# Performance work log

Hardware: AMD Instinct MI355X
Metric: run time of the kernel (lower is better)

Reference implementation:

```python
import jax, jax.numpy as jnp
import numpy as np
import math

GH, GW = 64, 64
FEAT_DIM = 32
NUM_COMP = 8
N = 1_000_000
H1, H2 = 128, 64
TWO_PI = 2.0 * math.pi
LN_EPS = 1e-5


def _layernorm(h, g, b):
    mu = jnp.mean(h, axis=-1, keepdims=True)
    var = jnp.var(h, axis=-1, keepdims=True)
    return (h - mu) * jax.lax.rsqrt(var + LN_EPS) * g + b


def setup_inputs() -> dict:
    key = jax.random.key(0)
    ks = jax.random.split(key, 8)
    coords = jax.random.uniform(ks[0], (N, 2), dtype=jnp.float32)
    feature_grid = jax.random.normal(ks[1], (GH, GW, FEAT_DIM), dtype=jnp.float32)
    d_in = 2 + FEAT_DIM
    W1 = jax.random.normal(ks[2], (d_in, H1), dtype=jnp.float32) / np.sqrt(d_in)
    b1 = jnp.zeros((H1,), jnp.float32)
    g1 = jnp.ones((H1,), jnp.float32)
    be1 = jnp.zeros((H1,), jnp.float32)
    W2 = jax.random.normal(ks[3], (H1, H2), dtype=jnp.float32) / np.sqrt(H1)
    b2 = jnp.zeros((H2,), jnp.float32)
    g2 = jnp.ones((H2,), jnp.float32)
    be2 = jnp.zeros((H2,), jnp.float32)
    W3 = jax.random.normal(ks[4], (H2, 6 * NUM_COMP), dtype=jnp.float32) / np.sqrt(H2)
    b3 = jnp.zeros((6 * NUM_COMP,), jnp.float32)
    return {"coords": coords, "feature_grid": feature_grid,
            "W1": W1, "b1": b1, "g1": g1, "be1": be1,
            "W2": W2, "b2": b2, "g2": g2, "be2": be2,
            "W3": W3, "b3": b3}


def reference(coords, feature_grid, W1, b1, g1, be1, W2, b2, g2, be2, W3, b3):
    # bilinear gather from feature grid
    x = coords[:, 0] * (GW - 1)
    y = coords[:, 1] * (GH - 1)
    x0 = jnp.clip(jnp.floor(x).astype(jnp.int32), 0, GW - 2)
    y0 = jnp.clip(jnp.floor(y).astype(jnp.int32), 0, GH - 2)
    x1 = x0 + 1
    y1 = y0 + 1
    dx = (x - x0.astype(jnp.float32))[:, None]
    dy = (y - y0.astype(jnp.float32))[:, None]
    f00 = feature_grid[y0, x0]  # [N, F]
    f01 = feature_grid[y1, x0]
    f10 = feature_grid[y0, x1]
    f11 = feature_grid[y1, x1]
    feat = ((1 - dx) * (1 - dy) * f00 + (1 - dx) * dy * f01
            + dx * (1 - dy) * f10 + dx * dy * f11)
    # MLP (dropout is identity in eval mode)
    h = jnp.concatenate([coords, feat], axis=-1)
    h = _layernorm(jax.nn.relu(h @ W1 + b1), g1, be1)
    h = _layernorm(jax.nn.relu(h @ W2 + b2), g2, be2)
    params = (h @ W3 + b3).reshape(-1, NUM_COMP, 6)
    # GMM parameter postprocessing
    weights = jax.nn.softmax(params[:, :, 0], axis=-1)
    speed = jax.nn.relu(params[:, :, 1])
    angle = jnp.mod(params[:, :, 2], TWO_PI)
    variances = jnp.exp(jnp.clip(params[:, :, 3:5], -10.0, 10.0))
    corr = 0.99 * jnp.tanh(params[:, :, 5])
    means = jnp.stack([speed, angle], axis=-1)
    gmm = jnp.concatenate([weights[..., None], means, variances, corr[..., None]], axis=-1)
    return (gmm, coords)
```

## Files before the change

kernel.cpp:

```cpp
#include <hip/hip_runtime.h>
#include <math.h>


constexpr int N_PTS = 1000000;
constexpr int GW = 64;
constexpr int FDIM = 32;
constexpr int DIN = 34;
constexpr int NH1 = 128;
constexpr int NH2 = 64;
constexpr int NOUT = 48;
constexpr int NC = 8;
constexpr int BLK = 128;

template<int N>
__device__ __forceinline__ float np_pairwise(const float* x) {
#pragma clang fp contract(off)
    float r[8];
#pragma unroll
    for (int j = 0; j < 8; ++j) r[j] = x[j];
#pragma unroll
    for (int m = 1; m < N / 8; ++m)
#pragma unroll
        for (int j = 0; j < 8; ++j) r[j] = r[j] + x[8 * m + j];
    return ((r[0] + r[1]) + (r[2] + r[3])) + ((r[4] + r[5]) + (r[6] + r[7]));
}

template<int N>
__device__ __forceinline__ float np_pairwise_sq(const float* x, float mu) {
#pragma clang fp contract(off)
    float r[8];
#pragma unroll
    for (int j = 0; j < 8; ++j) { const float d = x[j] - mu; r[j] = d * d; }
#pragma unroll
    for (int m = 1; m < N / 8; ++m)
#pragma unroll
        for (int j = 0; j < 8; ++j) {
            const float d = x[8 * m + j] - mu;
            r[j] = r[j] + d * d;
        }
    return ((r[0] + r[1]) + (r[2] + r[3])) + ((r[4] + r[5]) + (r[6] + r[7]));
}

__global__ __launch_bounds__(BLK, 2) void modgmm_np32(
    const float* __restrict__ coords,
    const float* __restrict__ grid,
    const float* __restrict__ W1, const float* __restrict__ b1,
    const float* __restrict__ g1, const float* __restrict__ be1,
    const float* __restrict__ W2, const float* __restrict__ b2,
    const float* __restrict__ g2, const float* __restrict__ be2,
    const float* __restrict__ W3, const float* __restrict__ b3,
    float* __restrict__ gmm_out, float* __restrict__ coords_out)
{
#pragma clang fp contract(off)
    __shared__ float sbuf[64 * BLK];
    const int tid = threadIdx.x;
    const int i = blockIdx.x * BLK + tid;
    if (i >= N_PTS) return;

    const float2 c2 = reinterpret_cast<const float2*>(coords)[i];
    const float cx = c2.x, cy = c2.y;

    const float x = cx * 63.0f;
    const float y = cy * 63.0f;
    int x0 = (int)floorf(x); x0 = x0 < 0 ? 0 : (x0 > 62 ? 62 : x0);
    int y0 = (int)floorf(y); y0 = y0 < 0 ? 0 : (y0 > 62 ? 62 : y0);
    const float dx = x - (float)x0;
    const float dy = y - (float)y0;
    const float omdx = 1.0f - dx;
    const float omdy = 1.0f - dy;
    const float w00 = omdx * omdy;
    const float w01 = omdx * dy;
    const float w10 = dx * omdy;
    const float w11 = dx * dy;

    const float* __restrict__ gp = grid + (y0 * GW + x0) * FDIM;

    sbuf[0 * BLK + tid] = cx;
    sbuf[1 * BLK + tid] = cy;
#pragma unroll
    for (int k = 0; k < FDIM; ++k) {
        const float t0 = w00 * gp[k];
        const float t1 = w01 * gp[GW * FDIM + k];
        const float t2 = w10 * gp[FDIM + k];
        const float t3 = w11 * gp[GW * FDIM + FDIM + k];
        sbuf[(2 + k) * BLK + tid] = ((t0 + t1) + t2) + t3;
    }

    float h[NH1];
#pragma unroll
    for (int j = 0; j < NH1; ++j) h[j] = 0.0f;
    for (int k = 0; k < DIN; ++k) {
        const float hv = sbuf[k * BLK + tid];
        const float* __restrict__ wr = W1 + k * NH1;
#pragma unroll
        for (int j = 0; j < NH1; ++j) h[j] = __builtin_fmaf(hv, wr[j], h[j]);
    }
#pragma unroll
    for (int j = 0; j < NH1; ++j) h[j] = fmaxf(h[j] + b1[j], 0.0f);

    {
        const float mu = np_pairwise<NH1>(h) / 128.0f;
        const float var = np_pairwise_sq<NH1>(h, mu) / 128.0f;
        const float rs = 1.0f / sqrtf(var + 1e-5f);
#pragma unroll
        for (int j = 0; j < NH1; ++j)
            h[j] = ((h[j] - mu) * rs) * g1[j] + be1[j];
    }

    float h2[NH2];
#pragma unroll
    for (int j = 0; j < NH2; ++j) h2[j] = 0.0f;
#pragma unroll
    for (int j = 0; j < 64; ++j) sbuf[j * BLK + tid] = h[j];
    for (int k = 0; k < 64; ++k) {
        const float hv = sbuf[k * BLK + tid];
        const float* __restrict__ wr = W2 + k * NH2;
#pragma unroll
        for (int j = 0; j < NH2; ++j) h2[j] = __builtin_fmaf(hv, wr[j], h2[j]);
    }
#pragma unroll
    for (int j = 0; j < 64; ++j) sbuf[j * BLK + tid] = h[64 + j];
    for (int k = 0; k < 64; ++k) {
        const float hv = sbuf[k * BLK + tid];
        const float* __restrict__ wr = W2 + (64 + k) * NH2;
#pragma unroll
        for (int j = 0; j < NH2; ++j) h2[j] = __builtin_fmaf(hv, wr[j], h2[j]);
    }
#pragma unroll
    for (int j = 0; j < NH2; ++j) h2[j] = fmaxf(h2[j] + b2[j], 0.0f);

    {
        const float mu = np_pairwise<NH2>(h2) / 64.0f;
        const float var = np_pairwise_sq<NH2>(h2, mu) / 64.0f;
        const float rs = 1.0f / sqrtf(var + 1e-5f);
#pragma unroll
        for (int j = 0; j < NH2; ++j)
            h2[j] = ((h2[j] - mu) * rs) * g2[j] + be2[j];
    }

    float o[NOUT];
#pragma unroll
    for (int j = 0; j < NOUT; ++j) o[j] = 0.0f;
#pragma unroll
    for (int j = 0; j < NH2; ++j) sbuf[j * BLK + tid] = h2[j];
    for (int k = 0; k < NH2; ++k) {
        const float hv = sbuf[k * BLK + tid];
        const float* __restrict__ wr = W3 + k * NOUT;
#pragma unroll
        for (int j = 0; j < NOUT; ++j) o[j] = __builtin_fmaf(hv, wr[j], o[j]);
    }
#pragma unroll
    for (int j = 0; j < NOUT; ++j) o[j] = o[j] + b3[j];

    const float TPf = 6.28318530717958647692f;
    float res[NOUT];
    float m = o[0];
#pragma unroll
    for (int c = 1; c < NC; ++c) m = fmaxf(m, o[6 * c]);
    float e[NC];
#pragma unroll
    for (int c = 0; c < NC; ++c) e[c] = expf(o[6 * c] - m);
    const float esum = ((e[0] + e[1]) + (e[2] + e[3])) + ((e[4] + e[5]) + (e[6] + e[7]));
#pragma unroll
    for (int c = 0; c < NC; ++c) {
        res[6 * c + 0] = e[c] / esum;
        res[6 * c + 1] = fmaxf(o[6 * c + 1], 0.0f);
        float a = fmodf(o[6 * c + 2], TPf);
        if (a < 0.0f) a += TPf;
        res[6 * c + 2] = a;
        res[6 * c + 3] = expf(fminf(fmaxf(o[6 * c + 3], -10.0f), 10.0f));
        res[6 * c + 4] = expf(fminf(fmaxf(o[6 * c + 4], -10.0f), 10.0f));
        res[6 * c + 5] = 0.99f * tanhf(o[6 * c + 5]);
    }

    float4* og = reinterpret_cast<float4*>(gmm_out + (size_t)i * NOUT);
#pragma unroll
    for (int q = 0; q < NOUT / 4; ++q)
        og[q] = make_float4(res[4 * q + 0], res[4 * q + 1], res[4 * q + 2], res[4 * q + 3]);
    reinterpret_cast<float2*>(coords_out)[i] = make_float2(cx, cy);
}

extern "C" void kernel_launch(void* const* d_in, const int* in_sizes, int n_in,
                              void* d_out, int out_size, void* d_ws, size_t ws_size,
                              hipStream_t stream) {
    const float* coords = (const float*)d_in[0];
    const float* grid   = (const float*)d_in[1];
    const float* W1  = (const float*)d_in[2];
    const float* b1  = (const float*)d_in[3];
    const float* g1  = (const float*)d_in[4];
    const float* be1 = (const float*)d_in[5];
    const float* W2  = (const float*)d_in[6];
    const float* b2  = (const float*)d_in[7];
    const float* g2  = (const float*)d_in[8];
    const float* be2 = (const float*)d_in[9];
    const float* W3  = (const float*)d_in[10];
    const float* b3  = (const float*)d_in[11];

    float* gmm_out    = (float*)d_out;
    float* coords_out = (float*)d_out + (size_t)N_PTS * NOUT;

    const int nblocks = (N_PTS + BLK - 1) / BLK;
    modgmm_np32<<<nblocks, BLK, 0, stream>>>(
        coords, grid, W1, b1, g1, be1, W2, b2, g2, be2, W3, b3,
        gmm_out, coords_out);
}
```

Baseline: 563.6 us.

## Split each point's MLP across four lanes with LDS exchange and shuffles

Each point is now handled by four lanes of the same wavefront. Every lane computes a quarter of each layer's outputs using float4 weight loads, writes it to LDS, and all four lanes read back the full row for the layer norm and the next layer. The softmax over the 8 components is finished with cross-lane xor shuffles. The goal is to cut per-thread register pressure (32/16/12 accumulators instead of 128/64/48) and so raise occupancy and latency hiding. In exchange, weight loads are no longer uniform across the wave, so they cannot use scalar loads. The layer-norm statistics are also recomputed redundantly by all four lanes, and the LDS exchange relies on wave-synchronous execution with no barrier.

```diff
diff --git a/kernel.cpp b/kernel.cpp
--- a/kernel.cpp
+++ b/kernel.cpp
@@ -9,39 +9,10 @@
 constexpr int NH1 = 128;
 constexpr int NH2 = 64;
 constexpr int NOUT = 48;
-constexpr int NC = 8;
-constexpr int BLK = 128;
-
-template<int N>
-__device__ __forceinline__ float np_pairwise(const float* x) {
-#pragma clang fp contract(off)
-    float r[8];
-#pragma unroll
-    for (int j = 0; j < 8; ++j) r[j] = x[j];
-#pragma unroll
-    for (int m = 1; m < N / 8; ++m)
-#pragma unroll
-        for (int j = 0; j < 8; ++j) r[j] = r[j] + x[8 * m + j];
-    return ((r[0] + r[1]) + (r[2] + r[3])) + ((r[4] + r[5]) + (r[6] + r[7]));
-}
-
-template<int N>
-__device__ __forceinline__ float np_pairwise_sq(const float* x, float mu) {
-#pragma clang fp contract(off)
-    float r[8];
-#pragma unroll
-    for (int j = 0; j < 8; ++j) { const float d = x[j] - mu; r[j] = d * d; }
-#pragma unroll
-    for (int m = 1; m < N / 8; ++m)
-#pragma unroll
-        for (int j = 0; j < 8; ++j) {
-            const float d = x[8 * m + j] - mu;
-            r[j] = r[j] + d * d;
-        }
-    return ((r[0] + r[1]) + (r[2] + r[3])) + ((r[4] + r[5]) + (r[6] + r[7]));
-}
-
-__global__ __launch_bounds__(BLK, 2) void modgmm_np32(
+constexpr int BLK = 256;
+constexpr int PTS = 64;
+
+__global__ __launch_bounds__(BLK, 4) void modgmm_np32_split4(
     const float* __restrict__ coords,
     const float* __restrict__ grid,
     const float* __restrict__ W1, const float* __restrict__ b1,
@@ -52,14 +23,16 @@
     float* __restrict__ gmm_out, float* __restrict__ coords_out)
 {
 #pragma clang fp contract(off)
-    __shared__ float sbuf[64 * BLK];
-    const int tid = threadIdx.x;
-    const int i = blockIdx.x * BLK + tid;
-    if (i >= N_PTS) return;
-
-    const float2 c2 = reinterpret_cast<const float2*>(coords)[i];
+    __shared__ float buf[NH1 * PTS];
+    const int tid  = threadIdx.x;
+    const int lane = tid & 63;
+    const int g    = lane >> 4;
+    const int pt   = ((tid >> 6) << 4) + (lane & 15);
+    const int gi   = blockIdx.x * PTS + pt;
+#define BUF(r) buf[(r) * PTS + pt]
+
+    const float2 c2 = reinterpret_cast<const float2*>(coords)[gi];
     const float cx = c2.x, cy = c2.y;
-
     const float x = cx * 63.0f;
     const float y = cy * 63.0f;
     int x0 = (int)floorf(x); x0 = x0 < 0 ? 0 : (x0 > 62 ? 62 : x0);
@@ -73,111 +46,215 @@
     const float w10 = dx * omdy;
     const float w11 = dx * dy;
 
-    const float* __restrict__ gp = grid + (y0 * GW + x0) * FDIM;
-
-    sbuf[0 * BLK + tid] = cx;
-    sbuf[1 * BLK + tid] = cy;
-#pragma unroll
-    for (int k = 0; k < FDIM; ++k) {
-        const float t0 = w00 * gp[k];
-        const float t1 = w01 * gp[GW * FDIM + k];
-        const float t2 = w10 * gp[FDIM + k];
-        const float t3 = w11 * gp[GW * FDIM + FDIM + k];
-        sbuf[(2 + k) * BLK + tid] = ((t0 + t1) + t2) + t3;
-    }
-
-    float h[NH1];
-#pragma unroll
-    for (int j = 0; j < NH1; ++j) h[j] = 0.0f;
+    if (g == 0) { BUF(0) = cx; BUF(1) = cy; }
+
+    {
+        const float* gp = grid + (y0 * GW + x0) * FDIM + g * 8;
+        const float4* q00 = reinterpret_cast<const float4*>(gp);
+        const float4* q01 = reinterpret_cast<const float4*>(gp + GW * FDIM);
+        const float4* q10 = reinterpret_cast<const float4*>(gp + FDIM);
+        const float4* q11 = reinterpret_cast<const float4*>(gp + GW * FDIM + FDIM);
+#pragma unroll
+        for (int e = 0; e < 2; ++e) {
+            const float4 a = q00[e], b = q01[e], c = q10[e], d = q11[e];
+            const int r = 2 + g * 8 + e * 4;
+            { const float t0 = w00*a.x, t1 = w01*b.x, t2 = w10*c.x, t3 = w11*d.x;
+              BUF(r+0) = ((t0 + t1) + t2) + t3; }
+            { const float t0 = w00*a.y, t1 = w01*b.y, t2 = w10*c.y, t3 = w11*d.y;
+              BUF(r+1) = ((t0 + t1) + t2) + t3; }
+            { const float t0 = w00*a.z, t1 = w01*b.z, t2 = w10*c.z, t3 = w11*d.z;
+              BUF(r+2) = ((t0 + t1) + t2) + t3; }
+            { const float t0 = w00*a.w, t1 = w01*b.w, t2 = w10*c.w, t3 = w11*d.w;
+              BUF(r+3) = ((t0 + t1) + t2) + t3; }
+        }
+    }
+
+    float acc[32];
+#pragma unroll
+    for (int jj = 0; jj < 32; ++jj) acc[jj] = 0.0f;
     for (int k = 0; k < DIN; ++k) {
-        const float hv = sbuf[k * BLK + tid];
-        const float* __restrict__ wr = W1 + k * NH1;
-#pragma unroll
-        for (int j = 0; j < NH1; ++j) h[j] = __builtin_fmaf(hv, wr[j], h[j]);
-    }
-#pragma unroll
-    for (int j = 0; j < NH1; ++j) h[j] = fmaxf(h[j] + b1[j], 0.0f);
-
-    {
-        const float mu = np_pairwise<NH1>(h) / 128.0f;
-        const float var = np_pairwise_sq<NH1>(h, mu) / 128.0f;
-        const float rs = 1.0f / sqrtf(var + 1e-5f);
-#pragma unroll
-        for (int j = 0; j < NH1; ++j)
-            h[j] = ((h[j] - mu) * rs) * g1[j] + be1[j];
-    }
-
-    float h2[NH2];
-#pragma unroll
-    for (int j = 0; j < NH2; ++j) h2[j] = 0.0f;
-#pragma unroll
-    for (int j = 0; j < 64; ++j) sbuf[j * BLK + tid] = h[j];
-    for (int k = 0; k < 64; ++k) {
-        const float hv = sbuf[k * BLK + tid];
-        const float* __restrict__ wr = W2 + k * NH2;
-#pragma unroll
-        for (int j = 0; j < NH2; ++j) h2[j] = __builtin_fmaf(hv, wr[j], h2[j]);
-    }
-#pragma unroll
-    for (int j = 0; j < 64; ++j) sbuf[j * BLK + tid] = h[64 + j];
-    for (int k = 0; k < 64; ++k) {
-        const float hv = sbuf[k * BLK + tid];
-        const float* __restrict__ wr = W2 + (64 + k) * NH2;
-#pragma unroll
-        for (int j = 0; j < NH2; ++j) h2[j] = __builtin_fmaf(hv, wr[j], h2[j]);
-    }
-#pragma unroll
-    for (int j = 0; j < NH2; ++j) h2[j] = fmaxf(h2[j] + b2[j], 0.0f);
-
-    {
-        const float mu = np_pairwise<NH2>(h2) / 64.0f;
-        const float var = np_pairwise_sq<NH2>(h2, mu) / 64.0f;
-        const float rs = 1.0f / sqrtf(var + 1e-5f);
-#pragma unroll
-        for (int j = 0; j < NH2; ++j)
-            h2[j] = ((h2[j] - mu) * rs) * g2[j] + be2[j];
-    }
-
-    float o[NOUT];
-#pragma unroll
-    for (int j = 0; j < NOUT; ++j) o[j] = 0.0f;
-#pragma unroll
-    for (int j = 0; j < NH2; ++j) sbuf[j * BLK + tid] = h2[j];
+        const float hv = BUF(k);
+        const float4* w4 = reinterpret_cast<const float4*>(W1 + k * NH1 + g * 32);
+#pragma unroll
+        for (int q = 0; q < 8; ++q) {
+            const float4 w = w4[q];
+            acc[4*q+0] = __builtin_fmaf(hv, w.x, acc[4*q+0]);
+            acc[4*q+1] = __builtin_fmaf(hv, w.y, acc[4*q+1]);
+            acc[4*q+2] = __builtin_fmaf(hv, w.z, acc[4*q+2]);
+            acc[4*q+3] = __builtin_fmaf(hv, w.w, acc[4*q+3]);
+        }
+    }
+    {
+        const float4* bv4 = reinterpret_cast<const float4*>(b1 + g * 32);
+#pragma unroll
+        for (int q = 0; q < 8; ++q) {
+            const float4 bv = bv4[q];
+            acc[4*q+0] = fmaxf(acc[4*q+0] + bv.x, 0.0f);
+            acc[4*q+1] = fmaxf(acc[4*q+1] + bv.y, 0.0f);
+            acc[4*q+2] = fmaxf(acc[4*q+2] + bv.z, 0.0f);
+            acc[4*q+3] = fmaxf(acc[4*q+3] + bv.w, 0.0f);
+        }
+#pragma unroll
+        for (int jj = 0; jj < 32; ++jj) BUF(g * 32 + jj) = acc[jj];
+    }
+
+    float mu1, rs1;
+    {
+        float r[8];
+#pragma unroll
+        for (int j = 0; j < 8; ++j) r[j] = BUF(j);
+#pragma unroll
+        for (int m = 1; m < 16; ++m)
+#pragma unroll
+            for (int j = 0; j < 8; ++j) r[j] = r[j] + BUF(8 * m + j);
+        mu1 = (((r[0]+r[1]) + (r[2]+r[3])) + ((r[4]+r[5]) + (r[6]+r[7]))) / 128.0f;
+#pragma unroll
+        for (int j = 0; j < 8; ++j) { const float d = BUF(j) - mu1; r[j] = d * d; }
+#pragma unroll
+        for (int m = 1; m < 16; ++m)
+#pragma unroll
+            for (int j = 0; j < 8; ++j) {
+                const float d = BUF(8 * m + j) - mu1;
+                r[j] = r[j] + d * d;
+            }
+        const float var = (((r[0]+r[1]) + (r[2]+r[3])) + ((r[4]+r[5]) + (r[6]+r[7]))) / 128.0f;
+        rs1 = 1.0f / sqrtf(var + 1e-5f);
+    }
+    {
+        const float4* gv4 = reinterpret_cast<const float4*>(g1 + g * 32);
+        const float4* ev4 = reinterpret_cast<const float4*>(be1 + g * 32);
+#pragma unroll
+        for (int q = 0; q < 8; ++q) {
+            const float4 gv = gv4[q], ev = ev4[q];
+            BUF(g*32 + 4*q+0) = ((acc[4*q+0] - mu1) * rs1) * gv.x + ev.x;
+            BUF(g*32 + 4*q+1) = ((acc[4*q+1] - mu1) * rs1) * gv.y + ev.y;
+            BUF(g*32 + 4*q+2) = ((acc[4*q+2] - mu1) * rs1) * gv.z + ev.z;
+            BUF(g*32 + 4*q+3) = ((acc[4*q+3] - mu1) * rs1) * gv.w + ev.w;
+        }
+    }
+
+    float acc2[16];
+#pragma unroll
+    for (int jj = 0; jj < 16; ++jj) acc2[jj] = 0.0f;
+    for (int k = 0; k < NH1; ++k) {
+        const float hv = BUF(k);
+        const float4* w4 = reinterpret_cast<const float4*>(W2 + k * NH2 + g * 16);
+#pragma unroll
+        for (int q = 0; q < 4; ++q) {
+            const float4 w = w4[q];
+            acc2[4*q+0] = __builtin_fmaf(hv, w.x, acc2[4*q+0]);
+            acc2[4*q+1] = __builtin_fmaf(hv, w.y, acc2[4*q+1]);
+            acc2[4*q+2] = __builtin_fmaf(hv, w.z, acc2[4*q+2]);
+            acc2[4*q+3] = __builtin_fmaf(hv, w.w, acc2[4*q+3]);
+        }
+    }
+    {
+        const float4* bv4 = reinterpret_cast<const float4*>(b2 + g * 16);
+#pragma unroll
+        for (int q = 0; q < 4; ++q) {
+            const float4 bv = bv4[q];
+            acc2[4*q+0] = fmaxf(acc2[4*q+0] + bv.x, 0.0f);
+            acc2[4*q+1] = fmaxf(acc2[4*q+1] + bv.y, 0.0f);
+            acc2[4*q+2] = fmaxf(acc2[4*q+2] + bv.z, 0.0f);
+            acc2[4*q+3] = fmaxf(acc2[4*q+3] + bv.w, 0.0f);
+        }
+#pragma unroll
+        for (int jj = 0; jj < 16; ++jj) BUF(g * 16 + jj) = acc2[jj];
+    }
+
+    float mu2, rs2;
+    {
+        float r[8];
+#pragma unroll
+        for (int j = 0; j < 8; ++j) r[j] = BUF(j);
+#pragma unroll
+        for (int m = 1; m < 8; ++m)
+#pragma unroll
+            for (int j = 0; j < 8; ++j) r[j] = r[j] + BUF(8 * m + j);
+        mu2 = (((r[0]+r[1]) + (r[2]+r[3])) + ((r[4]+r[5]) + (r[6]+r[7]))) / 64.0f;
+#pragma unroll
+        for (int j = 0; j < 8; ++j) { const float d = BUF(j) - mu2; r[j] = d * d; }
+#pragma unroll
+        for (int m = 1; m < 8; ++m)
+#pragma unroll
+            for (int j = 0; j < 8; ++j) {
+                const float d = BUF(8 * m + j) - mu2;
+                r[j] = r[j] + d * d;
+            }
+        const float var = (((r[0]+r[1]) + (r[2]+r[3])) + ((r[4]+r[5]) + (r[6]+r[7]))) / 64.0f;
+        rs2 = 1.0f / sqrtf(var + 1e-5f);
+    }
+    {
+        const float4* gv4 = reinterpret_cast<const float4*>(g2 + g * 16);
+        const float4* ev4 = reinterpret_cast<const float4*>(be2 + g * 16);
+#pragma unroll
+        for (int q = 0; q < 4; ++q) {
+            const float4 gv = gv4[q], ev = ev4[q];
+            BUF(g*16 + 4*q+0) = ((acc2[4*q+0] - mu2) * rs2) * gv.x + ev.x;
+            BUF(g*16 + 4*q+1) = ((acc2[4*q+1] - mu2) * rs2) * gv.y + ev.y;
+            BUF(g*16 + 4*q+2) = ((acc2[4*q+2] - mu2) * rs2) * gv.z + ev.z;
+            BUF(g*16 + 4*q+3) = ((acc2[4*q+3] - mu2) * rs2) * gv.w + ev.w;
+        }
+    }
+
+    float o[12];
+#pragma unroll
+    for (int jj = 0; jj < 12; ++jj) o[jj] = 0.0f;
     for (int k = 0; k < NH2; ++k) {
-        const float hv = sbuf[k * BLK + tid];
-        const float* __restrict__ wr = W3 + k * NOUT;
-#pragma unroll
-        for (int j = 0; j < NOUT; ++j) o[j] = __builtin_fmaf(hv, wr[j], o[j]);
-    }
-#pragma unroll
-    for (int j = 0; j < NOUT; ++j) o[j] = o[j] + b3[j];
+        const float hv = BUF(k);
+        const float4* w4 = reinterpret_cast<const float4*>(W3 + k * NOUT + g * 12);
+#pragma unroll
+        for (int q = 0; q < 3; ++q) {
+            const float4 w = w4[q];
+            o[4*q+0] = __builtin_fmaf(hv, w.x, o[4*q+0]);
+            o[4*q+1] = __builtin_fmaf(hv, w.y, o[4*q+1]);
+            o[4*q+2] = __builtin_fmaf(hv, w.z, o[4*q+2]);
+            o[4*q+3] = __builtin_fmaf(hv, w.w, o[4*q+3]);
+        }
+    }
+    {
+        const float4* bv4 = reinterpret_cast<const float4*>(b3 + g * 12);
+#pragma unroll
+        for (int q = 0; q < 3; ++q) {
+            const float4 bv = bv4[q];
+            o[4*q+0] = o[4*q+0] + bv.x;
+            o[4*q+1] = o[4*q+1] + bv.y;
+            o[4*q+2] = o[4*q+2] + bv.z;
+            o[4*q+3] = o[4*q+3] + bv.w;
+        }
+    }
 
     const float TPf = 6.28318530717958647692f;
-    float res[NOUT];
-    float m = o[0];
-#pragma unroll
-    for (int c = 1; c < NC; ++c) m = fmaxf(m, o[6 * c]);
-    float e[NC];
-#pragma unroll
-    for (int c = 0; c < NC; ++c) e[c] = expf(o[6 * c] - m);
-    const float esum = ((e[0] + e[1]) + (e[2] + e[3])) + ((e[4] + e[5]) + (e[6] + e[7]));
-#pragma unroll
-    for (int c = 0; c < NC; ++c) {
-        res[6 * c + 0] = e[c] / esum;
-        res[6 * c + 1] = fmaxf(o[6 * c + 1], 0.0f);
-        float a = fmodf(o[6 * c + 2], TPf);
+    float res[12];
+    float mp = fmaxf(o[0], o[6]);
+    mp = fmaxf(mp, __shfl_xor(mp, 16));
+    mp = fmaxf(mp, __shfl_xor(mp, 32));
+    const float e0 = expf(o[0] - mp);
+    const float e1 = expf(o[6] - mp);
+    const float s  = e0 + e1;
+    const float u  = s + __shfl_xor(s, 16);
+    const float esum = u + __shfl_xor(u, 32);
+    res[0] = e0 / esum;
+    res[6] = e1 / esum;
+#pragma unroll
+    for (int h = 0; h < 2; ++h) {
+        const int off = 6 * h;
+        res[off+1] = fmaxf(o[off+1], 0.0f);
+        float a = fmodf(o[off+2], TPf);
         if (a < 0.0f) a += TPf;
-        res[6 * c + 2] = a;
-        res[6 * c + 3] = expf(fminf(fmaxf(o[6 * c + 3], -10.0f), 10.0f));
-        res[6 * c + 4] = expf(fminf(fmaxf(o[6 * c + 4], -10.0f), 10.0f));
-        res[6 * c + 5] = 0.99f * tanhf(o[6 * c + 5]);
-    }
-
-    float4* og = reinterpret_cast<float4*>(gmm_out + (size_t)i * NOUT);
-#pragma unroll
-    for (int q = 0; q < NOUT / 4; ++q)
-        og[q] = make_float4(res[4 * q + 0], res[4 * q + 1], res[4 * q + 2], res[4 * q + 3]);
-    reinterpret_cast<float2*>(coords_out)[i] = make_float2(cx, cy);
+        res[off+2] = a;
+        res[off+3] = expf(fminf(fmaxf(o[off+3], -10.0f), 10.0f));
+        res[off+4] = expf(fminf(fmaxf(o[off+4], -10.0f), 10.0f));
+        res[off+5] = 0.99f * tanhf(o[off+5]);
+    }
+
+    float4* og = reinterpret_cast<float4*>(gmm_out + (size_t)gi * NOUT + g * 12);
+    og[0] = make_float4(res[0], res[1], res[2],  res[3]);
+    og[1] = make_float4(res[4], res[5], res[6],  res[7]);
+    og[2] = make_float4(res[8], res[9], res[10], res[11]);
+    if (g == 0)
+        reinterpret_cast<float2*>(coords_out)[gi] = make_float2(cx, cy);
+#undef BUF
 }
 
 extern "C" void kernel_launch(void* const* d_in, const int* in_sizes, int n_in,
@@ -199,8 +276,8 @@
     float* gmm_out    = (float*)d_out;
     float* coords_out = (float*)d_out + (size_t)N_PTS * NOUT;
 
-    const int nblocks = (N_PTS + BLK - 1) / BLK;
-    modgmm_np32<<<nblocks, BLK, 0, stream>>>(
+    const int nblocks = N_PTS / PTS;
+    modgmm_np32_split4<<<nblocks, BLK, 0, stream>>>(
         coords, grid, W1, b1, g1, be1, W2, b2, g2, be2, W3, b3,
         gmm_out, coords_out);
 }
```

After: 1.911 ms. 3.39x slower.

## Stage MLP weight matrices in LDS per block with vectorized reads

Applied to the files above, without the earlier changes.

Each block cooperatively copies W1, W2 and W3 into a 32KB shared buffer before each layer, separated by barriers, and reads weights as float4 from LDS instead of global memory. Out-of-range threads are clamped rather than returned early so that all threads reach the barriers. The aim is to cut repeated global or constant weight fetches. In exchange it doubles LDS use per block, adds barriers, and replaces uniform scalar loads with per-thread LDS reads.

```diff
diff --git a/kernel.cpp b/kernel.cpp
--- a/kernel.cpp
+++ b/kernel.cpp
@@ -41,7 +41,7 @@
     return ((r[0] + r[1]) + (r[2] + r[3])) + ((r[4] + r[5]) + (r[6] + r[7]));
 }
 
-__global__ __launch_bounds__(BLK, 2) void modgmm_np32(
+__global__ __launch_bounds__(BLK, 2) void modgmm_np32_ldsw(
     const float* __restrict__ coords,
     const float* __restrict__ grid,
     const float* __restrict__ W1, const float* __restrict__ b1,
@@ -53,9 +53,16 @@
 {
 #pragma clang fp contract(off)
     __shared__ float sbuf[64 * BLK];
+    __shared__ float wlds[8192];
     const int tid = threadIdx.x;
-    const int i = blockIdx.x * BLK + tid;
-    if (i >= N_PTS) return;
+    const int i_raw = blockIdx.x * BLK + tid;
+    const int i = i_raw < N_PTS ? i_raw : N_PTS - 1;
+
+    {
+        const float4* src = reinterpret_cast<const float4*>(W1);
+        float4* dst = reinterpret_cast<float4*>(wlds);
+        for (int idx = tid; idx < 1088; idx += BLK) dst[idx] = src[idx];
+    }
 
     const float2 c2 = reinterpret_cast<const float2*>(coords)[i];
     const float cx = c2.x, cy = c2.y;
@@ -86,14 +93,22 @@
         sbuf[(2 + k) * BLK + tid] = ((t0 + t1) + t2) + t3;
     }
 
+    __syncthreads();
+
     float h[NH1];
 #pragma unroll
     for (int j = 0; j < NH1; ++j) h[j] = 0.0f;
     for (int k = 0; k < DIN; ++k) {
         const float hv = sbuf[k * BLK + tid];
-        const float* __restrict__ wr = W1 + k * NH1;
-#pragma unroll
-        for (int j = 0; j < NH1; ++j) h[j] = __builtin_fmaf(hv, wr[j], h[j]);
+        const float* wr = wlds + k * NH1;
+#pragma unroll
+        for (int q = 0; q < NH1 / 4; ++q) {
+            const float4 w = *reinterpret_cast<const float4*>(wr + 4 * q);
+            h[4*q+0] = __builtin_fmaf(hv, w.x, h[4*q+0]);
+            h[4*q+1] = __builtin_fmaf(hv, w.y, h[4*q+1]);
+            h[4*q+2] = __builtin_fmaf(hv, w.z, h[4*q+2]);
+            h[4*q+3] = __builtin_fmaf(hv, w.w, h[4*q+3]);
+        }
     }
 #pragma unroll
     for (int j = 0; j < NH1; ++j) h[j] = fmaxf(h[j] + b1[j], 0.0f);
@@ -107,6 +122,14 @@
             h[j] = ((h[j] - mu) * rs) * g1[j] + be1[j];
     }
 
+    __syncthreads();
+    {
+        const float4* src = reinterpret_cast<const float4*>(W2);
+        float4* dst = reinterpret_cast<float4*>(wlds);
+        for (int idx = tid; idx < 2048; idx += BLK) dst[idx] = src[idx];
+    }
+    __syncthreads();
+
     float h2[NH2];
 #pragma unroll
     for (int j = 0; j < NH2; ++j) h2[j] = 0.0f;
@@ -114,17 +137,29 @@
     for (int j = 0; j < 64; ++j) sbuf[j * BLK + tid] = h[j];
     for (int k = 0; k < 64; ++k) {
         const float hv = sbuf[k * BLK + tid];
-        const float* __restrict__ wr = W2 + k * NH2;
-#pragma unroll
-        for (int j = 0; j < NH2; ++j) h2[j] = __builtin_fmaf(hv, wr[j], h2[j]);
+        const float* wr = wlds + k * NH2;
+#pragma unroll
+        for (int q = 0; q < NH2 / 4; ++q) {
+            const float4 w = *reinterpret_cast<const float4*>(wr + 4 * q);
+            h2[4*q+0] = __builtin_fmaf(hv, w.x, h2[4*q+0]);
+            h2[4*q+1] = __builtin_fmaf(hv, w.y, h2[4*q+1]);
+            h2[4*q+2] = __builtin_fmaf(hv, w.z, h2[4*q+2]);
+            h2[4*q+3] = __builtin_fmaf(hv, w.w, h2[4*q+3]);
+        }
     }
 #pragma unroll
     for (int j = 0; j < 64; ++j) sbuf[j * BLK + tid] = h[64 + j];
     for (int k = 0; k < 64; ++k) {
         const float hv = sbuf[k * BLK + tid];
-        const float* __restrict__ wr = W2 + (64 + k) * NH2;
-#pragma unroll
-        for (int j = 0; j < NH2; ++j) h2[j] = __builtin_fmaf(hv, wr[j], h2[j]);
+        const float* wr = wlds + (64 + k) * NH2;
+#pragma unroll
+        for (int q = 0; q < NH2 / 4; ++q) {
+            const float4 w = *reinterpret_cast<const float4*>(wr + 4 * q);
+            h2[4*q+0] = __builtin_fmaf(hv, w.x, h2[4*q+0]);
+            h2[4*q+1] = __builtin_fmaf(hv, w.y, h2[4*q+1]);
+            h2[4*q+2] = __builtin_fmaf(hv, w.z, h2[4*q+2]);
+            h2[4*q+3] = __builtin_fmaf(hv, w.w, h2[4*q+3]);
+        }
     }
 #pragma unroll
     for (int j = 0; j < NH2; ++j) h2[j] = fmaxf(h2[j] + b2[j], 0.0f);
@@ -138,6 +173,14 @@
             h2[j] = ((h2[j] - mu) * rs) * g2[j] + be2[j];
     }
 
+    __syncthreads();
+    {
+        const float4* src = reinterpret_cast<const float4*>(W3);
+        float4* dst = reinterpret_cast<float4*>(wlds);
+        for (int idx = tid; idx < 768; idx += BLK) dst[idx] = src[idx];
+    }
+    __syncthreads();
+
     float o[NOUT];
 #pragma unroll
     for (int j = 0; j < NOUT; ++j) o[j] = 0.0f;
@@ -145,9 +188,15 @@
     for (int j = 0; j < NH2; ++j) sbuf[j * BLK + tid] = h2[j];
     for (int k = 0; k < NH2; ++k) {
         const float hv = sbuf[k * BLK + tid];
-        const float* __restrict__ wr = W3 + k * NOUT;
-#pragma unroll
-        for (int j = 0; j < NOUT; ++j) o[j] = __builtin_fmaf(hv, wr[j], o[j]);
+        const float* wr = wlds + k * NOUT;
+#pragma unroll
+        for (int q = 0; q < NOUT / 4; ++q) {
+            const float4 w = *reinterpret_cast<const float4*>(wr + 4 * q);
+            o[4*q+0] = __builtin_fmaf(hv, w.x, o[4*q+0]);
+            o[4*q+1] = __builtin_fmaf(hv, w.y, o[4*q+1]);
+            o[4*q+2] = __builtin_fmaf(hv, w.z, o[4*q+2]);
+            o[4*q+3] = __builtin_fmaf(hv, w.w, o[4*q+3]);
+        }
     }
 #pragma unroll
     for (int j = 0; j < NOUT; ++j) o[j] = o[j] + b3[j];
@@ -173,11 +222,13 @@
         res[6 * c + 5] = 0.99f * tanhf(o[6 * c + 5]);
     }
 
-    float4* og = reinterpret_cast<float4*>(gmm_out + (size_t)i * NOUT);
-#pragma unroll
-    for (int q = 0; q < NOUT / 4; ++q)
-        og[q] = make_float4(res[4 * q + 0], res[4 * q + 1], res[4 * q + 2], res[4 * q + 3]);
-    reinterpret_cast<float2*>(coords_out)[i] = make_float2(cx, cy);
+    if (i_raw < N_PTS) {
+        float4* og = reinterpret_cast<float4*>(gmm_out + (size_t)i_raw * NOUT);
+#pragma unroll
+        for (int q = 0; q < NOUT / 4; ++q)
+            og[q] = make_float4(res[4 * q + 0], res[4 * q + 1], res[4 * q + 2], res[4 * q + 3]);
+        reinterpret_cast<float2*>(coords_out)[i_raw] = make_float2(cx, cy);
+    }
 }
 
 extern "C" void kernel_launch(void* const* d_in, const int* in_sizes, int n_in,
@@ -200,7 +251,7 @@
     float* coords_out = (float*)d_out + (size_t)N_PTS * NOUT;
 
     const int nblocks = (N_PTS + BLK - 1) / BLK;
-    modgmm_np32<<<nblocks, BLK, 0, stream>>>(
+    modgmm_np32_ldsw<<<nblocks, BLK, 0, stream>>>(
         coords, grid, W1, b1, g1, be1, W2, b2, g2, be2, W3, b3,
         gmm_out, coords_out);
 }
```

Result: slower. 1.440 ms (+155.5%).

## Chunk MLP output columns and double-buffer float4 weight loads

Applied to the files above, without the earlier changes.

Each of the three dense layers is restructured to compute output columns in chunks of 32 (or 24) accumulators, with weight rows loaded as float4 vectors and double-buffered so the next row's loads are issued before the current row's FMAs. This is meant to hide scalar/global weight load latency and cut register pressure from full-width accumulator arrays. In exchange the per-thread activations are reread from shared memory once per column chunk, and the extra prefetch registers may raise pressure.

```diff
diff --git a/kernel.cpp b/kernel.cpp
--- a/kernel.cpp
+++ b/kernel.cpp
@@ -41,7 +41,7 @@
     return ((r[0] + r[1]) + (r[2] + r[3])) + ((r[4] + r[5]) + (r[6] + r[7]));
 }
 
-__global__ __launch_bounds__(BLK, 2) void modgmm_np32(
+__global__ __launch_bounds__(BLK, 2) void modgmm_np32_pipe(
     const float* __restrict__ coords,
     const float* __restrict__ grid,
     const float* __restrict__ W1, const float* __restrict__ b1,
@@ -88,12 +88,43 @@
 
     float h[NH1];
 #pragma unroll
-    for (int j = 0; j < NH1; ++j) h[j] = 0.0f;
-    for (int k = 0; k < DIN; ++k) {
-        const float hv = sbuf[k * BLK + tid];
-        const float* __restrict__ wr = W1 + k * NH1;
-#pragma unroll
-        for (int j = 0; j < NH1; ++j) h[j] = __builtin_fmaf(hv, wr[j], h[j]);
+    for (int jc = 0; jc < 4; ++jc) {
+        const float* wbase = W1 + jc * 32;
+        float acc[32];
+#pragma unroll
+        for (int jj = 0; jj < 32; ++jj) acc[jj] = 0.0f;
+        float4 wa[8], wb[8];
+#pragma unroll
+        for (int q = 0; q < 8; ++q)
+            wa[q] = *reinterpret_cast<const float4*>(wbase + 4 * q);
+        for (int k = 0; k < DIN; k += 2) {
+            const float hv0 = sbuf[k * BLK + tid];
+            const float hv1 = sbuf[(k + 1) * BLK + tid];
+#pragma unroll
+            for (int q = 0; q < 8; ++q)
+                wb[q] = *reinterpret_cast<const float4*>(wbase + (k + 1) * NH1 + 4 * q);
+#pragma unroll
+            for (int q = 0; q < 8; ++q) {
+                acc[4*q+0] = __builtin_fmaf(hv0, wa[q].x, acc[4*q+0]);
+                acc[4*q+1] = __builtin_fmaf(hv0, wa[q].y, acc[4*q+1]);
+                acc[4*q+2] = __builtin_fmaf(hv0, wa[q].z, acc[4*q+2]);
+                acc[4*q+3] = __builtin_fmaf(hv0, wa[q].w, acc[4*q+3]);
+            }
+            if (k + 2 < DIN) {
+#pragma unroll
+                for (int q = 0; q < 8; ++q)
+                    wa[q] = *reinterpret_cast<const float4*>(wbase + (k + 2) * NH1 + 4 * q);
+            }
+#pragma unroll
+            for (int q = 0; q < 8; ++q) {
+                acc[4*q+0] = __builtin_fmaf(hv1, wb[q].x, acc[4*q+0]);
+                acc[4*q+1] = __builtin_fmaf(hv1, wb[q].y, acc[4*q+1]);
+                acc[4*q+2] = __builtin_fmaf(hv1, wb[q].z, acc[4*q+2]);
+                acc[4*q+3] = __builtin_fmaf(hv1, wb[q].w, acc[4*q+3]);
+            }
+        }
+#pragma unroll
+        for (int jj = 0; jj < 32; ++jj) h[jc * 32 + jj] = acc[jj];
     }
 #pragma unroll
     for (int j = 0; j < NH1; ++j) h[j] = fmaxf(h[j] + b1[j], 0.0f);
@@ -111,20 +142,48 @@
 #pragma unroll
     for (int j = 0; j < NH2; ++j) h2[j] = 0.0f;
 #pragma unroll
-    for (int j = 0; j < 64; ++j) sbuf[j * BLK + tid] = h[j];
-    for (int k = 0; k < 64; ++k) {
-        const float hv = sbuf[k * BLK + tid];
-        const float* __restrict__ wr = W2 + k * NH2;
-#pragma unroll
-        for (int j = 0; j < NH2; ++j) h2[j] = __builtin_fmaf(hv, wr[j], h2[j]);
-    }
-#pragma unroll
-    for (int j = 0; j < 64; ++j) sbuf[j * BLK + tid] = h[64 + j];
-    for (int k = 0; k < 64; ++k) {
-        const float hv = sbuf[k * BLK + tid];
-        const float* __restrict__ wr = W2 + (64 + k) * NH2;
-#pragma unroll
-        for (int j = 0; j < NH2; ++j) h2[j] = __builtin_fmaf(hv, wr[j], h2[j]);
+    for (int p = 0; p < 2; ++p) {
+#pragma unroll
+        for (int j = 0; j < 64; ++j) sbuf[j * BLK + tid] = h[p * 64 + j];
+#pragma unroll
+        for (int jc = 0; jc < 2; ++jc) {
+            const float* wbase = W2 + (size_t)(p * 64) * NH2 + jc * 32;
+            float acc[32];
+#pragma unroll
+            for (int jj = 0; jj < 32; ++jj) acc[jj] = h2[jc * 32 + jj];
+            float4 wa[8], wb[8];
+#pragma unroll
+            for (int q = 0; q < 8; ++q)
+                wa[q] = *reinterpret_cast<const float4*>(wbase + 4 * q);
+            for (int kk = 0; kk < 64; kk += 2) {
+                const float hv0 = sbuf[kk * BLK + tid];
+                const float hv1 = sbuf[(kk + 1) * BLK + tid];
+#pragma unroll
+                for (int q = 0; q < 8; ++q)
+                    wb[q] = *reinterpret_cast<const float4*>(wbase + (kk + 1) * NH2 + 4 * q);
+#pragma unroll
+                for (int q = 0; q < 8; ++q) {
+                    acc[4*q+0] = __builtin_fmaf(hv0, wa[q].x, acc[4*q+0]);
+                    acc[4*q+1] = __builtin_fmaf(hv0, wa[q].y, acc[4*q+1]);
+                    acc[4*q+2] = __builtin_fmaf(hv0, wa[q].z, acc[4*q+2]);
+                    acc[4*q+3] = __builtin_fmaf(hv0, wa[q].w, acc[4*q+3]);
+                }
+                if (kk + 2 < 64) {
+#pragma unroll
+                    for (int q = 0; q < 8; ++q)
+                        wa[q] = *reinterpret_cast<const float4*>(wbase + (kk + 2) * NH2 + 4 * q);
+                }
+#pragma unroll
+                for (int q = 0; q < 8; ++q) {
+                    acc[4*q+0] = __builtin_fmaf(hv1, wb[q].x, acc[4*q+0]);
+                    acc[4*q+1] = __builtin_fmaf(hv1, wb[q].y, acc[4*q+1]);
+                    acc[4*q+2] = __builtin_fmaf(hv1, wb[q].z, acc[4*q+2]);
+                    acc[4*q+3] = __builtin_fmaf(hv1, wb[q].w, acc[4*q+3]);
+                }
+            }
+#pragma unroll
+            for (int jj = 0; jj < 32; ++jj) h2[jc * 32 + jj] = acc[jj];
+        }
     }
 #pragma unroll
     for (int j = 0; j < NH2; ++j) h2[j] = fmaxf(h2[j] + b2[j], 0.0f);
@@ -138,16 +197,47 @@
             h2[j] = ((h2[j] - mu) * rs) * g2[j] + be2[j];
     }
 
+#pragma unroll
+    for (int j = 0; j < NH2; ++j) sbuf[j * BLK + tid] = h2[j];
     float o[NOUT];
 #pragma unroll
-    for (int j = 0; j < NOUT; ++j) o[j] = 0.0f;
-#pragma unroll
-    for (int j = 0; j < NH2; ++j) sbuf[j * BLK + tid] = h2[j];
-    for (int k = 0; k < NH2; ++k) {
-        const float hv = sbuf[k * BLK + tid];
-        const float* __restrict__ wr = W3 + k * NOUT;
-#pragma unroll
-        for (int j = 0; j < NOUT; ++j) o[j] = __builtin_fmaf(hv, wr[j], o[j]);
+    for (int jc = 0; jc < 2; ++jc) {
+        const float* wbase = W3 + jc * 24;
+        float acc[24];
+#pragma unroll
+        for (int jj = 0; jj < 24; ++jj) acc[jj] = 0.0f;
+        float4 wa[6], wb[6];
+#pragma unroll
+        for (int q = 0; q < 6; ++q)
+            wa[q] = *reinterpret_cast<const float4*>(wbase + 4 * q);
+        for (int k = 0; k < NH2; k += 2) {
+            const float hv0 = sbuf[k * BLK + tid];
+            const float hv1 = sbuf[(k + 1) * BLK + tid];
+#pragma unroll
+            for (int q = 0; q < 6; ++q)
+                wb[q] = *reinterpret_cast<const float4*>(wbase + (k + 1) * NOUT + 4 * q);
+#pragma unroll
+            for (int q = 0; q < 6; ++q) {
+                acc[4*q+0] = __builtin_fmaf(hv0, wa[q].x, acc[4*q+0]);
+                acc[4*q+1] = __builtin_fmaf(hv0, wa[q].y, acc[4*q+1]);
+                acc[4*q+2] = __builtin_fmaf(hv0, wa[q].z, acc[4*q+2]);
+                acc[4*q+3] = __builtin_fmaf(hv0, wa[q].w, acc[4*q+3]);
+            }
+            if (k + 2 < NH2) {
+#pragma unroll
+                for (int q = 0; q < 6; ++q)
+                    wa[q] = *reinterpret_cast<const float4*>(wbase + (k + 2) * NOUT + 4 * q);
+            }
+#pragma unroll
+            for (int q = 0; q < 6; ++q) {
+                acc[4*q+0] = __builtin_fmaf(hv1, wb[q].x, acc[4*q+0]);
+                acc[4*q+1] = __builtin_fmaf(hv1, wb[q].y, acc[4*q+1]);
+                acc[4*q+2] = __builtin_fmaf(hv1, wb[q].z, acc[4*q+2]);
+                acc[4*q+3] = __builtin_fmaf(hv1, wb[q].w, acc[4*q+3]);
+            }
+        }
+#pragma unroll
+        for (int jj = 0; jj < 24; ++jj) o[jc * 24 + jj] = acc[jj];
     }
 #pragma unroll
     for (int j = 0; j < NOUT; ++j) o[j] = o[j] + b3[j];
@@ -200,7 +290,7 @@
     float* coords_out = (float*)d_out + (size_t)N_PTS * NOUT;
 
     const int nblocks = (N_PTS + BLK - 1) / BLK;
-    modgmm_np32<<<nblocks, BLK, 0, stream>>>(
+    modgmm_np32_pipe<<<nblocks, BLK, 0, stream>>>(
         coords, grid, W1, b1, g1, be1, W2, b2, g2, be2, W3, b3,
         gmm_out, coords_out);
 }
```

Measured after the change: 1.865 ms. +230.9%, slower.
